# Performance work log

Hardware: AMD Instinct MI355X
Metric: run time of the kernel (lower is better)

## Reference

```python
import jax, jax.numpy as jnp
import numpy as np

D_MODEL = 1024
NUM_HEADS = 16
D_HEAD = D_MODEL // NUM_HEADS
MAX_DISTANCE = 128
SEQ_LEN = 2048


def setup_inputs() -> dict:
    key = jax.random.key(0)
    k_x, k_qkv, k_out, k_bias = jax.random.split(key, 4)
    scale = 1.0 / np.sqrt(D_MODEL)
    return {
        "x": jax.random.normal(k_x, (SEQ_LEN, D_MODEL), dtype=jnp.float32),
        "w_qkv": jax.random.normal(k_qkv, (D_MODEL, 3 * D_MODEL), dtype=jnp.float32) * scale,
        "w_out": jax.random.normal(k_out, (D_MODEL, D_MODEL), dtype=jnp.float32) * scale,
        "rel_bias": jax.random.normal(k_bias, (MAX_DISTANCE, NUM_HEADS), dtype=jnp.float32) * 0.02,
    }


def _position_bias(rel_bias, seq_len):
    # relative_position[q, k] = k - q; bucket = clip(|rel|, 0, max_distance-1)
    ctx = jnp.arange(seq_len)[:, None]
    mem = jnp.arange(seq_len)[None, :]
    bucket = jnp.clip(jnp.abs(mem - ctx), 0, MAX_DISTANCE - 1)  # [q, k]
    return rel_bias[bucket]  # [q, k, h]


def reference(x, w_qkv, w_out, rel_bias):
    seq_len = x.shape[0]
    qkv = x @ w_qkv  # [s, 3*d_model]
    q, k, v = jnp.split(qkv, 3, axis=-1)
    q = q.reshape(seq_len, NUM_HEADS, D_HEAD)
    k = k.reshape(seq_len, NUM_HEADS, D_HEAD)
    v = v.reshape(seq_len, NUM_HEADS, D_HEAD)
    bias = _position_bias(rel_bias, seq_len)  # [q, k, h]
    # flax dot_product_attention semantics: scale q by 1/sqrt(d_head), add bias, softmax over kv
    scores = jnp.einsum("qhd,khd->hqk", q, k) / jnp.sqrt(jnp.asarray(D_HEAD, q.dtype))
    scores = scores + jnp.transpose(bias, (2, 0, 1))  # [h, q, k]
    weights = jax.nn.softmax(scores, axis=-1)
    attn = jnp.einsum("hqk,khd->qhd", weights, v)  # [s, h, d_head]
    attn = attn.reshape(1, seq_len, D_MODEL)
    return attn @ w_out  # [1, s, d_model]
```

## Files before the change

### kernel.cpp

```cpp
#include <hip/hip_runtime.h>
#include <hip/hip_bf16.h>

#define SEQ   2048
#define DM    1024
#define NH    16
#define DH    64
#define MAXD  128

#define LOG2E 1.44269504f

typedef __attribute__((ext_vector_type(8))) short  short8;
typedef __attribute__((ext_vector_type(4))) float  float4v;

__device__ __forceinline__ short8 ld8(const void* p) {
    short8 v; __builtin_memcpy(&v, p, 16); return v;
}
__device__ __forceinline__ void st8(void* p, short8 v) {
    __builtin_memcpy(p, &v, 16);
}
__device__ __forceinline__ short bf16bits(float f) {
    __hip_bfloat16 b = __float2bfloat16(f);
    short s; __builtin_memcpy(&s, &b, 2); return s;
}
__device__ __forceinline__ float bits2f(short s) {
    unsigned u = (unsigned)(unsigned short)s << 16;
    return __builtin_bit_cast(float, u);
}
__device__ __forceinline__ unsigned packbf2(float a, float b) {
    unsigned ua = (__builtin_bit_cast(unsigned, a) + 0x8000u) >> 16;
    unsigned ub = (__builtin_bit_cast(unsigned, b) + 0x8000u) & 0xffff0000u;
    return ua | ub;
}
__device__ __forceinline__ unsigned packh2(float a, float b) {
    _Float16 ha = (_Float16)a, hb = (_Float16)b;
    unsigned short ua, ub;
    __builtin_memcpy(&ua, &ha, 2); __builtin_memcpy(&ub, &hb, 2);
    return (unsigned)ua | ((unsigned)ub << 16);
}
__device__ __forceinline__ float f16tof(short s) {
    _Float16 h; __builtin_memcpy(&h, &s, 2); return (float)h;
}
__device__ __forceinline__ float fexp2(float x) {
    float r; asm("v_exp_f32 %0, %1" : "=v"(r) : "v"(x)); return r;
}

__device__ __forceinline__ void async16(void* lds, const void* g) {
    __builtin_amdgcn_global_load_lds(
        (const __attribute__((address_space(1))) unsigned int*)g,
        (__attribute__((address_space(3))) unsigned int*)lds, 16, 0, 0);
}

__global__ __launch_bounds__(256) void prep_kernel(
    const float* __restrict__ wq, const float* __restrict__ wo,
    const float* __restrict__ x,
    __hip_bfloat16* __restrict__ wqT, __hip_bfloat16* __restrict__ woT,
    __hip_bfloat16* __restrict__ xb) {
    const int t = threadIdx.x;
    const int bx = blockIdx.x;
    if (bx >= 128) {
        const size_t id = (size_t)(bx - 128) * 32 + blockIdx.y;
        const size_t i  = id * 2048 + t * 8;
        float f[8]; __builtin_memcpy(f, x + i, 32);
        short8 v;
#pragma unroll
        for (int j = 0; j < 8; ++j) v[j] = bf16bits(f[j]);
        st8(xb + i, v);
        return;
    }
    __shared__ __hip_bfloat16 tile[32][33];
    const int tx = t % 32, ty = t / 32;
    const int r0 = blockIdx.y * 32;
    const float* src; __hip_bfloat16* dst; int ss, ds, c0;
    if (bx < 96) { src = wq; dst = wqT; ss = 3 * DM; ds = DM; c0 = bx * 32; }
    else         { src = wo; dst = woT; ss = DM;     ds = DM; c0 = (bx - 96) * 32; }
#pragma unroll
    for (int i = 0; i < 4; ++i)
        tile[ty + i * 8][tx] = __float2bfloat16(src[(size_t)(r0 + ty + i * 8) * ss + c0 + tx]);
    __syncthreads();
#pragma unroll
    for (int i = 0; i < 4; ++i)
        dst[(size_t)(c0 + ty + i * 8) * ds + r0 + tx] = tile[tx][ty + i * 8];
}

__global__ __launch_bounds__(256) void gemm_qkv(
    const __hip_bfloat16* __restrict__ A,
    const __hip_bfloat16* __restrict__ BT,
    __hip_bfloat16* __restrict__ C,
    __hip_bfloat16* __restrict__ vTg,
    int M, int N, int K) {
    __shared__ short As[2 * 128 * 32];
    __shared__ short Bs[2 * 64 * 32];
    __shared__ short Tv[64 * 132];

    const int t = threadIdx.x;
    const int w = t >> 6, lane = t & 63;
    const int l15 = lane & 15, quad = lane >> 4;
    const int row0 = blockIdx.y * 128;
    const int col0 = blockIdx.x * 64;
    const int wm = w >> 1, wn = w & 1;

    float4v acc[4][2];
#pragma unroll
    for (int i = 0; i < 4; ++i)
#pragma unroll
        for (int j = 0; j < 2; ++j) acc[i][j] = (float4v){0.f, 0.f, 0.f, 0.f};

    const int mloc0 = lane >> 2;
    const int u     = lane & 3;

    for (int k0 = 0; k0 < K; k0 += 64) {
#pragma unroll
        for (int kc = 0; kc < 2; ++kc) {
#pragma unroll
            for (int i = 0; i < 2; ++i) {
                const int c = 2 * w + i;
                async16(&As[kc * 4096 + c * 512],
                        A + (size_t)(row0 + c * 16 + mloc0) * K + k0 + kc * 32 + u * 8);
            }
            async16(&Bs[kc * 2048 + w * 512],
                    BT + (size_t)(col0 + w * 16 + mloc0) * K + k0 + kc * 32 + u * 8);
        }
        __syncthreads();

#pragma unroll
        for (int kc = 0; kc < 2; ++kc) {
            short8 af[4], bf[2];
#pragma unroll
            for (int mt = 0; mt < 4; ++mt)
                af[mt] = ld8(&As[kc * 4096 + (wm * 64 + mt * 16 + l15) * 32 + quad * 8]);
#pragma unroll
            for (int nt = 0; nt < 2; ++nt)
                bf[nt] = ld8(&Bs[kc * 2048 + (wn * 32 + nt * 16 + l15) * 32 + quad * 8]);
#pragma unroll
            for (int mt = 0; mt < 4; ++mt)
#pragma unroll
                for (int nt = 0; nt < 2; ++nt)
                    acc[mt][nt] = __builtin_amdgcn_mfma_f32_16x16x32_bf16(
                        af[mt], bf[nt], acc[mt][nt], 0, 0, 0);
        }
        __syncthreads();
    }

    if (col0 < 2 * DM) {
#pragma unroll
        for (int mt = 0; mt < 4; ++mt)
#pragma unroll
            for (int nt = 0; nt < 2; ++nt)
#pragma unroll
                for (int r = 0; r < 4; ++r) {
                    const int row = row0 + wm * 64 + mt * 16 + quad * 4 + r;
                    const int col = col0 + wn * 32 + nt * 16 + l15;
                    C[(size_t)row * N + col] = __float2bfloat16(acc[mt][nt][r]);
                }
    } else {
#pragma unroll
        for (int mt = 0; mt < 4; ++mt)
#pragma unroll
            for (int nt = 0; nt < 2; ++nt)
#pragma unroll
                for (int r = 0; r < 4; ++r)
                    Tv[(wn * 32 + nt * 16 + l15) * 132 + wm * 64 + mt * 16 + quad * 4 + r] =
                        bf16bits(acc[mt][nt][r]);
        __syncthreads();
#pragma unroll
        for (int p = 0; p < 4; ++p) {
            const int idx = p * 256 + t;
            const int dl = idx >> 4, uu = idx & 15;
            st8(&vTg[((size_t)(col0 - 2 * DM) + dl) * SEQ + row0 + uu * 8],
                ld8(&Tv[dl * 132 + uu * 8]));
        }
    }
}

__global__ __launch_bounds__(256) void gemm_out(
    const __hip_bfloat16* __restrict__ A,
    const __hip_bfloat16* __restrict__ BT,
    float* __restrict__ C,
    int M, int N, int K) {
    __shared__ short As[2 * 64 * 32];
    __shared__ short Bs[2 * 64 * 32];

    const int t = threadIdx.x;
    const int w = t >> 6, lane = t & 63;
    const int l15 = lane & 15, quad = lane >> 4;
    const int row0 = blockIdx.y * 64;
    const int col0 = blockIdx.x * 64;
    const int wm = w >> 1, wn = w & 1;

    float4v acc[2][2];
#pragma unroll
    for (int i = 0; i < 2; ++i)
#pragma unroll
        for (int j = 0; j < 2; ++j) acc[i][j] = (float4v){0.f, 0.f, 0.f, 0.f};

    const int mloc0 = lane >> 2;
    const int u     = lane & 3;

    for (int k0 = 0; k0 < K; k0 += 64) {
#pragma unroll
        for (int kc = 0; kc < 2; ++kc) {
            async16(&As[kc * 2048 + w * 512],
                    A + (size_t)(row0 + w * 16 + mloc0) * K + k0 + kc * 32 + u * 8);
            async16(&Bs[kc * 2048 + w * 512],
                    BT + (size_t)(col0 + w * 16 + mloc0) * K + k0 + kc * 32 + u * 8);
        }
        __syncthreads();

#pragma unroll
        for (int kc = 0; kc < 2; ++kc) {
            short8 af[2], bf[2];
#pragma unroll
            for (int mt = 0; mt < 2; ++mt)
                af[mt] = ld8(&As[kc * 2048 + (wm * 32 + mt * 16 + l15) * 32 + quad * 8]);
#pragma unroll
            for (int nt = 0; nt < 2; ++nt)
                bf[nt] = ld8(&Bs[kc * 2048 + (wn * 32 + nt * 16 + l15) * 32 + quad * 8]);
#pragma unroll
            for (int mt = 0; mt < 2; ++mt)
#pragma unroll
                for (int nt = 0; nt < 2; ++nt)
                    acc[mt][nt] = __builtin_amdgcn_mfma_f32_16x16x32_bf16(
                        af[mt], bf[nt], acc[mt][nt], 0, 0, 0);
        }
        __syncthreads();
    }

#pragma unroll
    for (int mt = 0; mt < 2; ++mt)
#pragma unroll
        for (int nt = 0; nt < 2; ++nt)
#pragma unroll
            for (int r = 0; r < 4; ++r) {
                const int row = row0 + wm * 32 + mt * 16 + quad * 4 + r;
                const int col = col0 + wn * 32 + nt * 16 + l15;
                C[(size_t)row * N + col] = acc[mt][nt][r];
            }
}

#define TK    128
#define NTILE (SEQ / 2 / TK)
#define KS    68
#define VS    132
#define PS    140

__global__ __launch_bounds__(256, 2) void attn_part(
    const __hip_bfloat16* __restrict__ qkv,
    const __hip_bfloat16* __restrict__ vT,
    const float* __restrict__ rel_bias,
    short* __restrict__ opart,
    float* __restrict__ ml) {
    __shared__ short KtP[4 * 32 * PS];
    __shared__ short Vt[DH * VS];
    __shared__ float biasL[MAXD];

    const int t = threadIdx.x;
    const int w = t >> 6, lane = t & 63;
    const int l15 = lane & 15, quad = lane >> 4;

    const int id = blockIdx.x;
    const int qb = (id >> 3) & 15;
    const int c  = (id & 7) + 8 * (id >> 7);
    const int h  = c & 15;
    const int half = c >> 4;
    const int kbase = half * (SEQ / 2);
    const int qw = qb * 128 + w * 32;

    if (t < MAXD) biasL[t] = rel_bias[t * NH + h] * LOG2E;

    short8 qf[2][2];
#pragma unroll
    for (int qg = 0; qg < 2; ++qg)
#pragma unroll
        for (int cc = 0; cc < 2; ++cc) {
            short8 raw = ld8(qkv + (size_t)(qw + qg * 16 + l15) * (3 * DM) + h * DH + cc * 32 + quad * 8);
#pragma unroll
            for (int j = 0; j < 8; ++j) qf[qg][cc][j] = bf16bits(bits2f(raw[j]) * (0.125f * LOG2E));
        }

    float4v o_acc[4][2];
#pragma unroll
    for (int nt = 0; nt < 4; ++nt)
#pragma unroll
        for (int qg = 0; qg < 2; ++qg) o_acc[nt][qg] = (float4v){0.f, 0.f, 0.f, 0.f};
    float m_i[2] = {-1e30f, -1e30f}, l_i[2] = {0.f, 0.f};

    short* Pw = &KtP[w * 32 * PS];

    for (int kb = 0; kb < NTILE; ++kb) {
        const int k0 = kbase + kb * TK;
#pragma unroll
        for (int p = 0; p < 4; ++p) {
            const int idx = p * 256 + t;
            const int row = idx >> 3, u = idx & 7;
            st8(&KtP[row * KS + u * 8],
                ld8(qkv + (size_t)(k0 + row) * (3 * DM) + DM + h * DH + u * 8));
        }
#pragma unroll
        for (int p = 0; p < 4; ++p) {
            const int idx = p * 256 + t;
            const int row = idx >> 4, u = idx & 15;
            st8(&Vt[row * VS + u * 8],
                ld8(vT + (size_t)(h * DH + row) * SEQ + k0 + u * 8));
        }
        __syncthreads();

        float4v s_acc[2][8];
#pragma unroll
        for (int qg = 0; qg < 2; ++qg)
#pragma unroll
            for (int kt = 0; kt < 8; ++kt) s_acc[qg][kt] = (float4v){0.f, 0.f, 0.f, 0.f};
#pragma unroll
        for (int cc = 0; cc < 2; ++cc)
#pragma unroll
            for (int kt = 0; kt < 8; ++kt) {
                short8 kf = ld8(&KtP[(kt * 16 + l15) * KS + (cc * 4 + quad) * 8]);
                s_acc[0][kt] = __builtin_amdgcn_mfma_f32_16x16x32_bf16(kf, qf[0][cc], s_acc[0][kt], 0, 0, 0);
                s_acc[1][kt] = __builtin_amdgcn_mfma_f32_16x16x32_bf16(kf, qf[1][cc], s_acc[1][kt], 0, 0, 0);
            }

        const int dlo = k0 - (qw + 31);
        const int dhi = qw - (k0 + TK - 1);
        if (dlo >= MAXD - 1 || dhi >= MAXD - 1) {
            const float bu = biasL[MAXD - 1];
#pragma unroll
            for (int qg = 0; qg < 2; ++qg)
#pragma unroll
                for (int kt = 0; kt < 8; ++kt)
#pragma unroll
                    for (int r = 0; r < 4; ++r) s_acc[qg][kt][r] += bu;
        } else {
#pragma unroll
            for (int qg = 0; qg < 2; ++qg) {
                const int qrow = qw + qg * 16 + l15;
#pragma unroll
                for (int kt = 0; kt < 8; ++kt)
#pragma unroll
                    for (int r = 0; r < 4; ++r) {
                        const int kg = k0 + kt * 16 + quad * 4 + r;
                        int rel = kg - qrow; if (rel < 0) rel = -rel;
                        if (rel > MAXD - 1) rel = MAXD - 1;
                        s_acc[qg][kt][r] += biasL[rel];
                    }
            }
        }

        float al[2];
#pragma unroll
        for (int qg = 0; qg < 2; ++qg) {
            float mk[8];
#pragma unroll
            for (int kt = 0; kt < 8; ++kt)
                mk[kt] = fmaxf(fmaxf(s_acc[qg][kt][0], s_acc[qg][kt][1]),
                               fmaxf(s_acc[qg][kt][2], s_acc[qg][kt][3]));
            float m = fmaxf(fmaxf(fmaxf(mk[0], mk[1]), fmaxf(mk[2], mk[3])),
                            fmaxf(fmaxf(mk[4], mk[5]), fmaxf(mk[6], mk[7])));
            m = fmaxf(m, __shfl_xor(m, 16, 64));
            m = fmaxf(m, __shfl_xor(m, 32, 64));
            const float mn = fmaxf(m_i[qg], m);
            al[qg] = fexp2(m_i[qg] - mn);
            m_i[qg] = mn;
            float sk[8];
#pragma unroll
            for (int kt = 0; kt < 8; ++kt) {
                float p0 = fexp2(s_acc[qg][kt][0] - mn);
                float p1 = fexp2(s_acc[qg][kt][1] - mn);
                float p2 = fexp2(s_acc[qg][kt][2] - mn);
                float p3 = fexp2(s_acc[qg][kt][3] - mn);
                s_acc[qg][kt][0] = p0; s_acc[qg][kt][1] = p1;
                s_acc[qg][kt][2] = p2; s_acc[qg][kt][3] = p3;
                sk[kt] = (p0 + p1) + (p2 + p3);
            }
            float rs = ((sk[0] + sk[1]) + (sk[2] + sk[3])) +
                       ((sk[4] + sk[5]) + (sk[6] + sk[7]));
            rs += __shfl_xor(rs, 16, 64);
            rs += __shfl_xor(rs, 32, 64);
            l_i[qg] = l_i[qg] * al[qg] + rs;
        }
#pragma unroll
        for (int nt = 0; nt < 4; ++nt)
#pragma unroll
            for (int qg = 0; qg < 2; ++qg)
#pragma unroll
                for (int r = 0; r < 4; ++r) o_acc[nt][qg][r] *= al[qg];

        __syncthreads();

#pragma unroll
        for (int qg = 0; qg < 2; ++qg)
#pragma unroll
            for (int kt = 0; kt < 8; ++kt) {
                unsigned d0 = packbf2(s_acc[qg][kt][0], s_acc[qg][kt][1]);
                unsigned d1 = packbf2(s_acc[qg][kt][2], s_acc[qg][kt][3]);
                unsigned long long v = (unsigned long long)d0 | ((unsigned long long)d1 << 32);
                __builtin_memcpy(&Pw[(qg * 16 + l15) * PS + kt * 16 + quad * 4], &v, 8);
            }

#pragma unroll
        for (int kc = 0; kc < 4; ++kc) {
            short8 pf0 = ld8(&Pw[l15 * PS + kc * 32 + quad * 8]);
            short8 pf1 = ld8(&Pw[(16 + l15) * PS + kc * 32 + quad * 8]);
#pragma unroll
            for (int nt = 0; nt < 4; ++nt) {
                short8 vf = ld8(&Vt[(nt * 16 + l15) * VS + kc * 32 + quad * 8]);
                o_acc[nt][0] = __builtin_amdgcn_mfma_f32_16x16x32_bf16(vf, pf0, o_acc[nt][0], 0, 0, 0);
                o_acc[nt][1] = __builtin_amdgcn_mfma_f32_16x16x32_bf16(vf, pf1, o_acc[nt][1], 0, 0, 0);
            }
        }
        __syncthreads();
    }

#pragma unroll
    for (int qg = 0; qg < 2; ++qg) {
        const float inv = 1.f / l_i[qg];
        const int qrow = qw + qg * 16 + l15;
#pragma unroll
        for (int nt = 0; nt < 4; ++nt) {
            unsigned d0 = packh2(o_acc[nt][qg][0] * inv, o_acc[nt][qg][1] * inv);
            unsigned d1 = packh2(o_acc[nt][qg][2] * inv, o_acc[nt][qg][3] * inv);
            unsigned long long v = (unsigned long long)d0 | ((unsigned long long)d1 << 32);
            __builtin_memcpy(opart + ((size_t)half * SEQ + qrow) * DM + h * DH + nt * 16 + quad * 4, &v, 8);
        }
    }
    if (quad == 0) {
#pragma unroll
        for (int qg = 0; qg < 2; ++qg) {
            const int qrow = qw + qg * 16 + l15;
            float* mp = ml + (((size_t)half * SEQ + qrow) * NH + h) * 2;
            mp[0] = m_i[qg];
            mp[1] = l_i[qg];
        }
    }
}

__global__ __launch_bounds__(256) void combine_kernel(
    const short* __restrict__ opart,
    const float* __restrict__ ml,
    __hip_bfloat16* __restrict__ attnb) {
    const size_t e = ((size_t)blockIdx.x * 256 + threadIdx.x) * 8;
    const int row = (int)(e >> 10);
    const int c0  = (int)(e & 1023);
    const int h   = c0 >> 6;

    const float* mp1 = ml + ((size_t)row * NH + h) * 2;
    const float* mp2 = mp1 + (size_t)SEQ * NH * 2;
    const float m1 = mp1[0], l1 = mp1[1];
    const float m2 = mp2[0], l2 = mp2[1];
    const float mx = fmaxf(m1, m2);
    const float e1 = fexp2(m1 - mx) * l1;
    const float e2 = fexp2(m2 - mx) * l2;
    const float inv = 1.f / (e1 + e2);
    const float w1 = e1 * inv, w2 = e2 * inv;

    short8 a = ld8(opart + (size_t)row * DM + c0);
    short8 b = ld8(opart + (size_t)SEQ * DM + (size_t)row * DM + c0);
    short8 o;
#pragma unroll
    for (int j = 0; j < 8; ++j)
        o[j] = bf16bits(w1 * f16tof(a[j]) + w2 * f16tof(b[j]));
    st8(attnb + (size_t)row * DM + c0, o);
}

extern "C" void kernel_launch(void* const* d_in, const int* in_sizes, int n_in,
                              void* d_out, int out_size, void* d_ws, size_t ws_size,
                              hipStream_t stream) {
    const float* x        = (const float*)d_in[0];
    const float* w_qkv    = (const float*)d_in[1];
    const float* w_out    = (const float*)d_in[2];
    const float* rel_bias = (const float*)d_in[3];
    float* out = (float*)d_out;

    char* p = (char*)d_ws;
    __hip_bfloat16* xb    = (__hip_bfloat16*)p;  p += (size_t)SEQ * DM * 2;
    __hip_bfloat16* wqT   = (__hip_bfloat16*)p;  p += (size_t)3 * DM * DM * 2;
    __hip_bfloat16* woT   = (__hip_bfloat16*)p;  p += (size_t)DM * DM * 2;
    __hip_bfloat16* qkvb  = (__hip_bfloat16*)p;  p += (size_t)SEQ * 3 * DM * 2;
    __hip_bfloat16* vT    = (__hip_bfloat16*)p;  p += (size_t)DM * SEQ * 2;
    __hip_bfloat16* attnb = (__hip_bfloat16*)p;

    short* opart = (short*)d_ws;
    float* ml    = (float*)((char*)d_ws + (size_t)2 * SEQ * DM * 2);

    prep_kernel<<<dim3(160, 32), 256, 0, stream>>>(w_qkv, w_out, x, wqT, woT, xb);

    gemm_qkv<<<dim3(3 * DM / 64, SEQ / 128), 256, 0, stream>>>(
        xb, wqT, qkvb, vT, SEQ, 3 * DM, DM);

    attn_part<<<512, 256, 0, stream>>>(qkvb, vT, rel_bias, opart, ml);
    combine_kernel<<<1024, 256, 0, stream>>>(opart, ml, attnb);

    gemm_out<<<dim3(DM / 64, SEQ / 64), 256, 0, stream>>>(
        attnb, woT, out, SEQ, DM, DM);
}
```

Before: 153.1 us.

## Enlarge QKV GEMM tile to 128x128 with XOR-swizzled shared memory layout

The QKV projection GEMM now uses 128x128 output tiles instead of 128x64, so each wave computes a 64x64 sub-tile with a 4x4 MFMA grid and more operand reuse per shared-memory load. The shared-memory layout changes to 64-wide K rows with an XOR swizzle on 16-byte chunks to avoid bank conflicts. The buffer is reused for the V transpose epilogue, which now runs in two halves. The grid drops to 384 blocks, which lowers occupancy and raises register pressure from the larger accumulator array.

```diff
diff --git a/kernel.cpp b/kernel.cpp
--- a/kernel.cpp
+++ b/kernel.cpp
@@ -88,53 +88,56 @@
     __hip_bfloat16* __restrict__ C,
     __hip_bfloat16* __restrict__ vTg,
     int M, int N, int K) {
-    __shared__ short As[2 * 128 * 32];
-    __shared__ short Bs[2 * 64 * 32];
-    __shared__ short Tv[64 * 132];
+    __shared__ short Smem[2 * 128 * 64];
+    short* As = Smem;
+    short* Bs = Smem + 128 * 64;
 
     const int t = threadIdx.x;
     const int w = t >> 6, lane = t & 63;
     const int l15 = lane & 15, quad = lane >> 4;
     const int row0 = blockIdx.y * 128;
-    const int col0 = blockIdx.x * 64;
+    const int col0 = blockIdx.x * 128;
     const int wm = w >> 1, wn = w & 1;
 
-    float4v acc[4][2];
+    float4v acc[4][4];
 #pragma unroll
     for (int i = 0; i < 4; ++i)
 #pragma unroll
-        for (int j = 0; j < 2; ++j) acc[i][j] = (float4v){0.f, 0.f, 0.f, 0.f};
-
-    const int mloc0 = lane >> 2;
-    const int u     = lane & 3;
+        for (int j = 0; j < 4; ++j) acc[i][j] = (float4v){0.f, 0.f, 0.f, 0.f};
+
+    const int rowoff  = w * 8 + (lane >> 3);
+    const int lanecol = (((lane & 7) ^ ((lane >> 3) & 7)) << 4);
+    const char* ap = (const char*)A  + ((size_t)(row0 + rowoff) * K) * 2 + lanecol;
+    const char* bp = (const char*)BT + ((size_t)(col0 + rowoff) * K) * 2 + lanecol;
+
+    const int swr = (l15 & 7) << 4;
 
     for (int k0 = 0; k0 < K; k0 += 64) {
 #pragma unroll
+        for (int p = 0; p < 4; ++p)
+            async16(&As[p * 2048 + w * 512], ap + (size_t)p * 32 * K * 2 + k0 * 2);
+#pragma unroll
+        for (int p = 0; p < 4; ++p)
+            async16(&Bs[p * 2048 + w * 512], bp + (size_t)p * 32 * K * 2 + k0 * 2);
+        __syncthreads();
+
+#pragma unroll
         for (int kc = 0; kc < 2; ++kc) {
-#pragma unroll
-            for (int i = 0; i < 2; ++i) {
-                const int c = 2 * w + i;
-                async16(&As[kc * 4096 + c * 512],
-                        A + (size_t)(row0 + c * 16 + mloc0) * K + k0 + kc * 32 + u * 8);
-            }
-            async16(&Bs[kc * 2048 + w * 512],
-                    BT + (size_t)(col0 + w * 16 + mloc0) * K + k0 + kc * 32 + u * 8);
-        }
-        __syncthreads();
-
-#pragma unroll
-        for (int kc = 0; kc < 2; ++kc) {
-            short8 af[4], bf[2];
+            short8 af[4], bf[4];
+#pragma unroll
+            for (int mt = 0; mt < 4; ++mt) {
+                const int ra = wm * 64 + mt * 16 + l15;
+                af[mt] = ld8((const char*)As + ra * 128 + ((kc * 64 + quad * 16) ^ swr));
+            }
+#pragma unroll
+            for (int nt = 0; nt < 4; ++nt) {
+                const int rb = wn * 64 + nt * 16 + l15;
+                bf[nt] = ld8((const char*)Bs + rb * 128 + ((kc * 64 + quad * 16) ^ swr));
+            }
 #pragma unroll
             for (int mt = 0; mt < 4; ++mt)
-                af[mt] = ld8(&As[kc * 4096 + (wm * 64 + mt * 16 + l15) * 32 + quad * 8]);
-#pragma unroll
-            for (int nt = 0; nt < 2; ++nt)
-                bf[nt] = ld8(&Bs[kc * 2048 + (wn * 32 + nt * 16 + l15) * 32 + quad * 8]);
-#pragma unroll
-            for (int mt = 0; mt < 4; ++mt)
-#pragma unroll
-                for (int nt = 0; nt < 2; ++nt)
+#pragma unroll
+                for (int nt = 0; nt < 4; ++nt)
                     acc[mt][nt] = __builtin_amdgcn_mfma_f32_16x16x32_bf16(
                         af[mt], bf[nt], acc[mt][nt], 0, 0, 0);
         }
@@ -145,29 +148,36 @@
 #pragma unroll
         for (int mt = 0; mt < 4; ++mt)
 #pragma unroll
-            for (int nt = 0; nt < 2; ++nt)
+            for (int nt = 0; nt < 4; ++nt)
 #pragma unroll
                 for (int r = 0; r < 4; ++r) {
                     const int row = row0 + wm * 64 + mt * 16 + quad * 4 + r;
-                    const int col = col0 + wn * 32 + nt * 16 + l15;
+                    const int col = col0 + wn * 64 + nt * 16 + l15;
                     C[(size_t)row * N + col] = __float2bfloat16(acc[mt][nt][r]);
                 }
     } else {
-#pragma unroll
-        for (int mt = 0; mt < 4; ++mt)
-#pragma unroll
-            for (int nt = 0; nt < 2; ++nt)
-#pragma unroll
-                for (int r = 0; r < 4; ++r)
-                    Tv[(wn * 32 + nt * 16 + l15) * 132 + wm * 64 + mt * 16 + quad * 4 + r] =
-                        bf16bits(acc[mt][nt][r]);
-        __syncthreads();
-#pragma unroll
-        for (int p = 0; p < 4; ++p) {
-            const int idx = p * 256 + t;
-            const int dl = idx >> 4, uu = idx & 15;
-            st8(&vTg[((size_t)(col0 - 2 * DM) + dl) * SEQ + row0 + uu * 8],
-                ld8(&Tv[dl * 132 + uu * 8]));
+        short* Tv = Smem;
+#pragma unroll
+        for (int H = 0; H < 2; ++H) {
+            if (wn == H) {
+#pragma unroll
+                for (int mt = 0; mt < 4; ++mt)
+#pragma unroll
+                    for (int nt = 0; nt < 4; ++nt)
+#pragma unroll
+                        for (int r = 0; r < 4; ++r)
+                            Tv[(nt * 16 + l15) * 132 + wm * 64 + mt * 16 + quad * 4 + r] =
+                                bf16bits(acc[mt][nt][r]);
+            }
+            __syncthreads();
+#pragma unroll
+            for (int p = 0; p < 4; ++p) {
+                const int idx = p * 256 + t;
+                const int dl = idx >> 4, uu = idx & 15;
+                st8(&vTg[((size_t)(col0 - 2 * DM) + H * 64 + dl) * SEQ + row0 + uu * 8],
+                    ld8(&Tv[dl * 132 + uu * 8]));
+            }
+            __syncthreads();
         }
     }
 }
@@ -482,7 +492,7 @@
 
     prep_kernel<<<dim3(160, 32), 256, 0, stream>>>(w_qkv, w_out, x, wqT, woT, xb);
 
-    gemm_qkv<<<dim3(3 * DM / 64, SEQ / 128), 256, 0, stream>>>(
+    gemm_qkv<<<dim3(3 * DM / 128, SEQ / 128), 256, 0, stream>>>(
         xb, wqT, qkvb, vT, SEQ, 3 * DM, DM);
 
     attn_part<<<512, 256, 0, stream>>>(qkvb, vT, rel_bias, opart, ml);
```

Measured after the change: 153.9 us. No clear change (+0.6%).
